# Performance work log

Measured on AMD Instinct MI355X. Metric: run time of the kernel, lower is better.

## Reference

```python
import jax, jax.numpy as jnp
import numpy as np

BETA_MAX = 5.0


def setup_inputs() -> dict:
    key = jax.random.key(0)
    ks = jax.random.split(key, 10)
    N, M, R, d, NTAU, G = 100000, 1000000, 4, 16, 16, 128
    return {
        "c_3": jax.random.randint(ks[0], (M,), 0, N),
        "u_3": jax.random.randint(ks[1], (M,), 0, N),
        "v_3": jax.random.randint(ks[2], (M,), 0, N),
        "t_tau": jax.random.randint(ks[3], (M,), 0, NTAU),
        "batch": jnp.sort(jax.random.randint(ks[4], (N,), 0, G)),
        "Q3": jax.random.normal(ks[5], (N, R, d), dtype=jnp.float32),
        "K3": jax.random.normal(ks[6], (N, R, d), dtype=jnp.float32),
        "T_params": jax.random.normal(ks[7], (NTAU, d), dtype=jnp.float32),
        "raw_lambda_3": jax.random.uniform(ks[8], (1,), dtype=jnp.float32),
        "raw_beta_3": jax.random.uniform(ks[9], (1,), dtype=jnp.float32),
        "num_nodes": N,
        "num_graphs": G,
    }


def reference(c_3, u_3, v_3, t_tau, batch, Q3, K3, T_params,
              raw_lambda_3, raw_beta_3, num_nodes, num_graphs):
    R, d = Q3.shape[-2], Q3.shape[-1]
    scale = (R * d) ** 0.5
    lam = jax.nn.softplus(raw_lambda_3[0])            # positive_param
    beta = jnp.minimum(jax.nn.softplus(raw_beta_3[0]), BETA_MAX)  # inverse_temperature

    # fused motif dot: gather Q/K by triangle indices, contract over d -> [M, R]
    T_sel = T_params[t_tau]                           # [M, d]
    ell = jnp.einsum('mrd,mrd,mrd,md->mr', Q3[c_3], K3[u_3], K3[v_3], T_sel) / scale
    z = beta * ell                                    # [M, R]

    # segment logsumexp over center-node segments c_3 -> [num_nodes, R]
    seg_max = jax.ops.segment_max(z, c_3, num_segments=num_nodes)
    safe_max = jnp.where(jnp.isfinite(seg_max), seg_max, 0.0)
    sums = jax.ops.segment_sum(jnp.exp(z - safe_max[c_3]), c_3, num_segments=num_nodes)
    lse = jnp.where(sums > 0, safe_max + jnp.log(jnp.where(sums > 0, sums, 1.0)), 0.0)

    # scatter-add node lse into graphs -> [num_graphs, R]
    graph_lse = jax.ops.segment_sum(lse, batch, num_segments=num_graphs)
    return (lam / beta) * graph_lse
```

## Files before the change

kernel.cpp:

```cpp
#include <hip/hip_runtime.h>


#define RR 4
#define DD 16
#define BETA_MAX 5.0f

typedef float v2f __attribute__((ext_vector_type(2)));
typedef float v4f __attribute__((ext_vector_type(4)));

#if defined(__has_builtin)
#if __has_builtin(__builtin_nontemporal_load)
#define NT_LOAD(p) __builtin_nontemporal_load(p)
#else
#define NT_LOAD(p) (*(p))
#endif
#else
#define NT_LOAD(p) (*(p))
#endif

__device__ __forceinline__ float softplus_f(float x) {
    return log1pf(__expf(x));
}

__device__ __forceinline__ int pack4_fp8(v4f f) {
    int w = 0;
    w = __builtin_amdgcn_cvt_pk_fp8_f32(f.x, f.y, w, false);
    w = __builtin_amdgcn_cvt_pk_fp8_f32(f.z, f.w, w, true);
    return w;
}

__global__ void me_init_convert(const float* __restrict__ raw_lam,
                                const float* __restrict__ raw_beta,
                                const float* __restrict__ Q3,
                                const float* __restrict__ K3,
                                int* __restrict__ Q8, int* __restrict__ K8,
                                float* __restrict__ scal, float* __restrict__ sums,
                                float* __restrict__ out,
                                int n4each, int nr, int out_size) {
    int i = blockIdx.x * blockDim.x + threadIdx.x;
    if (i == 0) {
        float beta = fminf(softplus_f(raw_beta[0]), BETA_MAX);
        float lam  = softplus_f(raw_lam[0]);
        scal[0] = beta * 0.125f;
        scal[1] = lam / beta;
    }
    if (i < nr) sums[i] = 0.0f;
    if (i < out_size) out[i] = 0.0f;
    if (i < 2 * n4each) {
        const float* src = (i < n4each) ? Q3 : K3;
        int*         dst = (i < n4each) ? Q8 : K8;
        int j = (i < n4each) ? i : i - n4each;
        v4f f = NT_LOAD((const v4f*)src + j);
        dst[j] = pack4_fp8(f);
    }
}

__device__ __forceinline__ float dot16_fp8(int4 q8, int4 u8, int4 v8,
                                           const float* __restrict__ Trow) {
    float acc = 0.0f;
    const int qw[4] = {q8.x, q8.y, q8.z, q8.w};
    const int uw[4] = {u8.x, u8.y, u8.z, u8.w};
    const int vw[4] = {v8.x, v8.y, v8.z, v8.w};
#pragma unroll
    for (int j = 0; j < 4; ++j) {
        v2f ql = __builtin_amdgcn_cvt_pk_f32_fp8(qw[j], false);
        v2f qh = __builtin_amdgcn_cvt_pk_f32_fp8(qw[j], true);
        v2f ul = __builtin_amdgcn_cvt_pk_f32_fp8(uw[j], false);
        v2f uh = __builtin_amdgcn_cvt_pk_f32_fp8(uw[j], true);
        v2f vl = __builtin_amdgcn_cvt_pk_f32_fp8(vw[j], false);
        v2f vh = __builtin_amdgcn_cvt_pk_f32_fp8(vw[j], true);
        const v4f tw = *(const v4f*)(Trow + 4 * j);
        acc += ql.x * ul.x * vl.x * tw.x + ql.y * ul.y * vl.y * tw.y +
               qh.x * uh.x * vh.x * tw.z + qh.y * uh.y * vh.y * tw.w;
    }
    return acc;
}

__global__ __launch_bounds__(256)
void me_motif_8(const int* __restrict__ c3, const int* __restrict__ u3,
                const int* __restrict__ v3, const int* __restrict__ tt,
                const int4* __restrict__ Q8, const int4* __restrict__ K8,
                const float* __restrict__ Tp, const float* __restrict__ scal,
                float* __restrict__ sums, int M, int half) {
    int tid = blockIdx.x * blockDim.x + threadIdx.x;
    int m0 = tid >> 2;
    if (m0 >= half) return;
    int k = tid & 3;
    int m1 = m0 + half;
    bool has1 = (m1 < M);
    int m1c = has1 ? m1 : m0;

    int c0 = NT_LOAD(c3 + m0);
    int u0 = NT_LOAD(u3 + m0);
    int v0 = NT_LOAD(v3 + m0);
    int t0 = NT_LOAD(tt + m0);
    int c1 = NT_LOAD(c3 + m1c);
    int u1 = NT_LOAD(u3 + m1c);
    int v1 = NT_LOAD(v3 + m1c);
    int t1 = NT_LOAD(tt + m1c);

    float bscale = scal[0];

    int4 q0 = Q8[(size_t)c0 * 4 + k];
    int4 a0 = K8[(size_t)u0 * 4 + k];
    int4 b0 = K8[(size_t)v0 * 4 + k];
    int4 q1 = Q8[(size_t)c1 * 4 + k];
    int4 a1 = K8[(size_t)u1 * 4 + k];
    int4 b1 = K8[(size_t)v1 * 4 + k];

    float p0 = dot16_fp8(q0, a0, b0, Tp + (size_t)t0 * DD);
    float p1 = dot16_fp8(q1, a1, b1, Tp + (size_t)t1 * DD);

    atomicAdd(&sums[c0 * RR + k], __expf(bscale * p0));
    if (has1) atomicAdd(&sums[c1 * RR + k], __expf(bscale * p1));
}

__global__ void me_motif_f32(const int* __restrict__ c3, const int* __restrict__ u3,
                             const int* __restrict__ v3, const int* __restrict__ tt,
                             const float* __restrict__ Q3, const float* __restrict__ K3,
                             const float* __restrict__ Tp, const float* __restrict__ scal,
                             float* __restrict__ sums, int M) {
    int tid = blockIdx.x * blockDim.x + threadIdx.x;
    int m = tid >> 4;
    if (m >= M) return;
    int l = tid & 15;
    int r = l >> 2;
    int off = r * DD + ((l & 3) << 2);
    int dc  = (l & 3) << 2;

    int c = c3[m], u = u3[m], v = v3[m], t = tt[m];
    float bscale = scal[0];

    const float4 q  = *(const float4*)(Q3 + ((size_t)c * (RR * DD) + off));
    const float4 ku = *(const float4*)(K3 + ((size_t)u * (RR * DD) + off));
    const float4 kv = *(const float4*)(K3 + ((size_t)v * (RR * DD) + off));
    const float4 tw = *(const float4*)(Tp + ((size_t)t * DD + dc));

    float p = q.x * ku.x * kv.x * tw.x + q.y * ku.y * kv.y * tw.y +
              q.z * ku.z * kv.z * tw.z + q.w * ku.w * kv.w * tw.w;
    p += __shfl_xor(p, 1);
    p += __shfl_xor(p, 2);

    if ((l & 3) == 0) atomicAdd(&sums[c * RR + r], __expf(bscale * p));
}

__global__ void me_init_f32(const float* __restrict__ raw_lam,
                            const float* __restrict__ raw_beta,
                            float* __restrict__ scal, float* __restrict__ sums,
                            float* __restrict__ out, int nr, int out_size) {
    int i = blockIdx.x * blockDim.x + threadIdx.x;
    if (i == 0) {
        float beta = fminf(softplus_f(raw_beta[0]), BETA_MAX);
        float lam  = softplus_f(raw_lam[0]);
        scal[0] = beta * 0.125f;
        scal[1] = lam / beta;
    }
    if (i < nr) sums[i] = 0.0f;
    if (i < out_size) out[i] = 0.0f;
}

__global__ void me_node(const float* __restrict__ sums, const int* __restrict__ batch,
                        const float* __restrict__ scal, float* __restrict__ out,
                        int N, int out_size) {
    extern __shared__ float acc[];
    for (int i = threadIdx.x; i < out_size; i += blockDim.x) acc[i] = 0.0f;
    __syncthreads();

    for (int n = blockIdx.x * blockDim.x + threadIdx.x; n < N;
         n += gridDim.x * blockDim.x) {
        v4f s = *((const v4f*)sums + n);
        int g = batch[n] * RR;
        if (s.x > 0.0f) atomicAdd(&acc[g + 0], logf(s.x));
        if (s.y > 0.0f) atomicAdd(&acc[g + 1], logf(s.y));
        if (s.z > 0.0f) atomicAdd(&acc[g + 2], logf(s.z));
        if (s.w > 0.0f) atomicAdd(&acc[g + 3], logf(s.w));
    }
    __syncthreads();

    float coef = scal[1];
    for (int i = threadIdx.x; i < out_size; i += blockDim.x) {
        float a = acc[i];
        if (a != 0.0f) atomicAdd(&out[i], a * coef);
    }
}

extern "C" void kernel_launch(void* const* d_in, const int* in_sizes, int n_in,
                              void* d_out, int out_size, void* d_ws, size_t ws_size,
                              hipStream_t stream) {
    const int*   c3    = (const int*)d_in[0];
    const int*   u3    = (const int*)d_in[1];
    const int*   v3    = (const int*)d_in[2];
    const int*   tt    = (const int*)d_in[3];
    const int*   batch = (const int*)d_in[4];
    const float* Q3    = (const float*)d_in[5];
    const float* K3    = (const float*)d_in[6];
    const float* Tp    = (const float*)d_in[7];
    const float* rlam  = (const float*)d_in[8];
    const float* rbeta = (const float*)d_in[9];

    const int M   = in_sizes[0];
    const int nel = in_sizes[5];
    const int N   = nel / (RR * DD);
    const int nr  = N * RR;

    const size_t fp8_bytes = (size_t)nel;
    const size_t need = 2 * fp8_bytes + (4 + (size_t)nr) * sizeof(float);

    float* out = (float*)d_out;

    if (ws_size >= need) {
        int*   Q8   = (int*)d_ws;
        int*   K8   = (int*)((char*)d_ws + fp8_bytes);
        float* scal = (float*)((char*)d_ws + 2 * fp8_bytes);
        float* sums = scal + 4;

        const int n4each = nel / 4;
        {
            int tot = 2 * n4each;
            if (nr > tot) tot = nr;
            if (out_size > tot) tot = out_size;
            me_init_convert<<<(tot + 255) / 256, 256, 0, stream>>>(
                rlam, rbeta, Q3, K3, Q8, K8, scal, sums, out, n4each, nr, out_size);
        }
        {
            const int half = (M + 1) / 2;
            long long threads = (long long)half * 4;
            int blocks = (int)((threads + 255) / 256);
            me_motif_8<<<blocks, 256, 0, stream>>>(c3, u3, v3, tt, (const int4*)Q8,
                                                   (const int4*)K8, Tp, scal, sums,
                                                   M, half);
        }
        {
            int nblk = (N + 255) / 256;
            if (nblk > 256) nblk = 256;
            me_node<<<nblk, 256, (size_t)out_size * sizeof(float), stream>>>(
                sums, batch, scal, out, N, out_size);
        }
    } else {
        float* scal = (float*)d_ws;
        float* sums = scal + 4;
        {
            int tot = nr > out_size ? nr : out_size;
            me_init_f32<<<(tot + 255) / 256, 256, 0, stream>>>(rlam, rbeta, scal, sums, out, nr, out_size);
        }
        {
            long long threads = (long long)M * 16;
            int blocks = (int)((threads + 255) / 256);
            me_motif_f32<<<blocks, 256, 0, stream>>>(c3, u3, v3, tt, Q3, K3, Tp, scal, sums, M);
        }
        {
            int nblk = (N + 255) / 256;
            if (nblk > 256) nblk = 256;
            me_node<<<nblk, 256, (size_t)out_size * sizeof(float), stream>>>(
                sums, batch, scal, out, N, out_size);
        }
    }
}
```

Baseline: 180.6 us.

## Process four motifs per thread and stage pre-scaled T table in LDS

Each thread now handles four triangle motifs instead of two, giving more independent gathers in flight per thread and using half as many threads overall. The 16x16 T_params table is loaded into shared memory once per block with the beta scale folded in, so the per-motif multiply by bscale disappears and T rows are read from LDS instead of global memory. The costs are a block-wide barrier and more registers per thread, which may lower occupancy. The LDS load of Tp[threadIdx.x] also assumes 256 threads per block and a table of exactly NTAU*d = 256 floats.

New measurement: 182.2 us. About the same (+0.9%).

```diff
diff --git a/kernel.cpp b/kernel.cpp
--- a/kernel.cpp
+++ b/kernel.cpp
@@ -56,7 +56,7 @@
 }
 
 __device__ __forceinline__ float dot16_fp8(int4 q8, int4 u8, int4 v8,
-                                           const float* __restrict__ Trow) {
+                                           const float* Trow) {
     float acc = 0.0f;
     const int qw[4] = {q8.x, q8.y, q8.z, q8.w};
     const int uw[4] = {u8.x, u8.y, u8.z, u8.w};
@@ -81,25 +81,31 @@
                 const int* __restrict__ v3, const int* __restrict__ tt,
                 const int4* __restrict__ Q8, const int4* __restrict__ K8,
                 const float* __restrict__ Tp, const float* __restrict__ scal,
-                float* __restrict__ sums, int M, int half) {
+                float* __restrict__ sums, int M, int quarter) {
+    __shared__ float Tl[256];
+    {
+        float bscale = scal[0];
+        Tl[threadIdx.x] = Tp[threadIdx.x] * bscale;
+    }
+    __syncthreads();
+
     int tid = blockIdx.x * blockDim.x + threadIdx.x;
     int m0 = tid >> 2;
-    if (m0 >= half) return;
+    if (m0 >= quarter) return;
     int k = tid & 3;
-    int m1 = m0 + half;
-    bool has1 = (m1 < M);
-    int m1c = has1 ? m1 : m0;
-
-    int c0 = NT_LOAD(c3 + m0);
-    int u0 = NT_LOAD(u3 + m0);
-    int v0 = NT_LOAD(v3 + m0);
-    int t0 = NT_LOAD(tt + m0);
-    int c1 = NT_LOAD(c3 + m1c);
-    int u1 = NT_LOAD(u3 + m1c);
-    int v1 = NT_LOAD(v3 + m1c);
-    int t1 = NT_LOAD(tt + m1c);
-
-    float bscale = scal[0];
+
+    int m1 = m0 + quarter, m2 = m0 + 2 * quarter, m3 = m0 + 3 * quarter;
+    bool h1 = (m1 < M), h2 = (m2 < M), h3 = (m3 < M);
+    int m1c = h1 ? m1 : m0, m2c = h2 ? m2 : m0, m3c = h3 ? m3 : m0;
+
+    int c0 = NT_LOAD(c3 + m0),  u0 = NT_LOAD(u3 + m0);
+    int v0 = NT_LOAD(v3 + m0),  t0 = NT_LOAD(tt + m0);
+    int c1 = NT_LOAD(c3 + m1c), u1 = NT_LOAD(u3 + m1c);
+    int v1 = NT_LOAD(v3 + m1c), t1 = NT_LOAD(tt + m1c);
+    int c2 = NT_LOAD(c3 + m2c), u2 = NT_LOAD(u3 + m2c);
+    int v2 = NT_LOAD(v3 + m2c), t2 = NT_LOAD(tt + m2c);
+    int c3i = NT_LOAD(c3 + m3c), u3i = NT_LOAD(u3 + m3c);
+    int v3i = NT_LOAD(v3 + m3c), t3 = NT_LOAD(tt + m3c);
 
     int4 q0 = Q8[(size_t)c0 * 4 + k];
     int4 a0 = K8[(size_t)u0 * 4 + k];
@@ -107,12 +113,22 @@
     int4 q1 = Q8[(size_t)c1 * 4 + k];
     int4 a1 = K8[(size_t)u1 * 4 + k];
     int4 b1 = K8[(size_t)v1 * 4 + k];
-
-    float p0 = dot16_fp8(q0, a0, b0, Tp + (size_t)t0 * DD);
-    float p1 = dot16_fp8(q1, a1, b1, Tp + (size_t)t1 * DD);
-
-    atomicAdd(&sums[c0 * RR + k], __expf(bscale * p0));
-    if (has1) atomicAdd(&sums[c1 * RR + k], __expf(bscale * p1));
+    int4 q2 = Q8[(size_t)c2 * 4 + k];
+    int4 a2 = K8[(size_t)u2 * 4 + k];
+    int4 b2 = K8[(size_t)v2 * 4 + k];
+    int4 q3 = Q8[(size_t)c3i * 4 + k];
+    int4 a3 = K8[(size_t)u3i * 4 + k];
+    int4 b3 = K8[(size_t)v3i * 4 + k];
+
+    float p0 = dot16_fp8(q0, a0, b0, &Tl[t0 * DD]);
+    float p1 = dot16_fp8(q1, a1, b1, &Tl[t1 * DD]);
+    float p2 = dot16_fp8(q2, a2, b2, &Tl[t2 * DD]);
+    float p3 = dot16_fp8(q3, a3, b3, &Tl[t3 * DD]);
+
+    atomicAdd(&sums[c0 * RR + k], __expf(p0));
+    if (h1) atomicAdd(&sums[c1 * RR + k], __expf(p1));
+    if (h2) atomicAdd(&sums[c2 * RR + k], __expf(p2));
+    if (h3) atomicAdd(&sums[c3i * RR + k], __expf(p3));
 }
 
 __global__ void me_motif_f32(const int* __restrict__ c3, const int* __restrict__ u3,
@@ -223,12 +239,12 @@
                 rlam, rbeta, Q3, K3, Q8, K8, scal, sums, out, n4each, nr, out_size);
         }
         {
-            const int half = (M + 1) / 2;
-            long long threads = (long long)half * 4;
+            const int quarter = (M + 3) / 4;
+            long long threads = (long long)quarter * 4;
             int blocks = (int)((threads + 255) / 256);
             me_motif_8<<<blocks, 256, 0, stream>>>(c3, u3, v3, tt, (const int4*)Q8,
                                                    (const int4*)K8, Tp, scal, sums,
-                                                   M, half);
+                                                   M, quarter);
         }
         {
             int nblk = (N + 255) / 256;
```
